# Optimization experiments

Measured on AMD Instinct MI355X. Metric: run time of the kernel, lower is better.

Reference implementation:

```python
import jax, jax.numpy as jnp
import numpy as np

NUM_HEADS = 16


def setup_inputs() -> dict:
    key = jax.random.key(0)
    ks = jax.random.split(key, 5)
    B, S, D = 2, 2048, 1024
    scale = 1.0 / np.sqrt(D)
    return {
        "hidden_states": jax.random.normal(ks[0], (B, S, D), dtype=jnp.float32),
        "Wq": jax.random.normal(ks[1], (D, D), dtype=jnp.float32) * scale,
        "bq": jnp.zeros((D,), jnp.float32),
        "Wk": jax.random.normal(ks[2], (D, D), dtype=jnp.float32) * scale,
        "bk": jnp.zeros((D,), jnp.float32),
        "Wv": jax.random.normal(ks[3], (D, D), dtype=jnp.float32) * scale,
        "bv": jnp.zeros((D,), jnp.float32),
        "Wo": jax.random.normal(ks[4], (D, D), dtype=jnp.float32) * scale,
        "bo": jnp.zeros((D,), jnp.float32),
    }


def reference(hidden_states, Wq, bq, Wk, bk, Wv, bv, Wo, bo):
    B, S, D = hidden_states.shape
    H = NUM_HEADS
    Dh = D // H

    def split_heads(x):  # [B,S,D] -> [B,H,S,Dh]
        return x.reshape(B, S, H, Dh).transpose(0, 2, 1, 3)

    q = split_heads(hidden_states @ Wq + bq)
    k = split_heads(hidden_states @ Wk + bk)
    v = split_heads(hidden_states @ Wv + bv)

    # causal additive mask: -inf strictly above the diagonal (triu, diagonal=1)
    i = jnp.arange(S)
    causal = jnp.where(i[None, :] > i[:, None], -jnp.inf, 0.0).astype(hidden_states.dtype)  # [S,S]

    scores = jnp.einsum("bhsd,bhtd->bhst", q, k) / jnp.sqrt(jnp.asarray(Dh, hidden_states.dtype))
    scores = scores + causal[None, None, :, :]
    weights = jax.nn.softmax(scores, axis=-1)  # [B,H,S,S]
    ctx = jnp.einsum("bhst,bhtd->bhsd", weights, v)
    ctx = ctx.transpose(0, 2, 1, 3).reshape(B, S, D)
    return ctx @ Wo + bo
```

## Files before the change

kernel.cpp:

```cpp
#include <hip/hip_runtime.h>
#include <math.h>

#define SEQ    2048
#define DMODEL 1024
#define NHEADS 16
#define DHEAD  64
#define NBATCH 2

typedef __attribute__((ext_vector_type(8)))  short bf16x8;
typedef __attribute__((ext_vector_type(4)))  float f32x4;
typedef __attribute__((ext_vector_type(16))) float f32x16;

__device__ __forceinline__ unsigned short f2bf(float f) {
    union { float f; unsigned u; } v; v.f = f;
    unsigned r = (v.u + 0x7FFF + ((v.u >> 16) & 1)) >> 16;
    return (unsigned short)r;
}

__device__ __forceinline__ unsigned cvt_pk_bf16(float lo, float hi) {
    unsigned r;
    asm("v_cvt_pk_bf16_f32 %0, %1, %2" : "=v"(r) : "v"(lo), "v"(hi));
    return r;
}

__device__ __forceinline__ void gload16(const void* g, void* l) {
    __builtin_amdgcn_global_load_lds(
        (const __attribute__((address_space(1))) unsigned*)g,
        (__attribute__((address_space(3))) unsigned*)l, 16, 0, 0);
}

__global__ __launch_bounds__(256)
void cast_bf16_kernel(const float* __restrict__ in, unsigned short* __restrict__ out) {
    const size_t g8 = ((size_t)blockIdx.x * 256 + threadIdx.x) * 8;
    float4 a = *reinterpret_cast<const float4*>(in + g8);
    float4 b = *reinterpret_cast<const float4*>(in + g8 + 4);
    bf16x8 o;
    o[0] = (short)f2bf(a.x); o[1] = (short)f2bf(a.y);
    o[2] = (short)f2bf(a.z); o[3] = (short)f2bf(a.w);
    o[4] = (short)f2bf(b.x); o[5] = (short)f2bf(b.y);
    o[6] = (short)f2bf(b.z); o[7] = (short)f2bf(b.w);
    *reinterpret_cast<bf16x8*>(out + g8) = o;
}

__global__ __launch_bounds__(256)
void wt_cast4_kernel(const float* __restrict__ W0, const float* __restrict__ W1,
                     const float* __restrict__ W2, const float* __restrict__ W3,
                     unsigned short* __restrict__ out) {
    __shared__ float tile[64][65];
    const int wsel = blockIdx.y;
    const float* W = (wsel == 0) ? W0 : (wsel == 1) ? W1 : (wsel == 2) ? W2 : W3;
    unsigned short* Wt = out + (size_t)wsel * 1024 * 1024;

    const int nt  = blockIdx.x & 15;
    const int kt  = blockIdx.x >> 4;
    const int tid = threadIdx.x;

#pragma unroll
    for (int r = 0; r < 4; ++r) {
        int kl = r * 16 + (tid >> 4);
        int nl = (tid & 15) * 4;
        float4 v = *reinterpret_cast<const float4*>(
            &W[(size_t)(kt * 64 + kl) * 1024 + nt * 64 + nl]);
        tile[kl][nl + 0] = v.x; tile[kl][nl + 1] = v.y;
        tile[kl][nl + 2] = v.z; tile[kl][nl + 3] = v.w;
    }
    __syncthreads();

    const int n  = tid >> 2;
    const int kc = (tid & 3) * 16;
    bf16x8 o0, o1;
#pragma unroll
    for (int i = 0; i < 8; ++i) o0[i] = (short)f2bf(tile[kc + i][n]);
#pragma unroll
    for (int i = 0; i < 8; ++i) o1[i] = (short)f2bf(tile[kc + 8 + i][n]);
    unsigned short* op = Wt + (size_t)(nt * 64 + n) * 1024 + kt * 64 + kc;
    *reinterpret_cast<bf16x8*>(op)     = o0;
    *reinterpret_cast<bf16x8*>(op + 8) = o1;
}

__global__ __launch_bounds__(256)
void vt_kernel(const unsigned short* __restrict__ Vh, unsigned short* __restrict__ Vt) {
    __shared__ unsigned short tile[64][72];
    const int bid = blockIdx.x;
    const int st  = bid & 31;
    const int bh  = bid >> 5;
    const int s0  = st * 64;
    const int tid = threadIdx.x;

    const int sl = tid >> 2;
    const int dc = (tid & 3) * 16;
    const unsigned short* src = Vh + ((size_t)bh * SEQ + s0 + sl) * 64 + dc;
    *reinterpret_cast<bf16x8*>(&tile[sl][dc])     = *reinterpret_cast<const bf16x8*>(src);
    *reinterpret_cast<bf16x8*>(&tile[sl][dc + 8]) = *reinterpret_cast<const bf16x8*>(src + 8);
    __syncthreads();

    const int dl = tid >> 2;
    const int sc = (tid & 3) * 16;
    unsigned short tmp[16];
#pragma unroll
    for (int k2 = 0; k2 < 16; ++k2) tmp[k2] = tile[sc + k2][dl];
    unsigned short* dst = Vt + ((size_t)bh * 64 + dl) * SEQ + s0 + sc;
    *reinterpret_cast<bf16x8*>(dst)     = *reinterpret_cast<bf16x8*>(&tmp[0]);
    *reinterpret_cast<bf16x8*>(dst + 8) = *reinterpret_cast<bf16x8*>(&tmp[8]);
}

template <int MODE>
__global__ __launch_bounds__(256)
void gemm_bf16(const unsigned short* __restrict__ A,
               const unsigned short* __restrict__ Bt,
               const float* __restrict__ bias0, const float* __restrict__ bias1,
               const float* __restrict__ bias2,
               float* __restrict__ Cf,
               unsigned short* __restrict__ Qo, unsigned short* __restrict__ Ko,
               unsigned short* __restrict__ Vo,
               int M, int N, int K) {
    __shared__ unsigned short As[2][128 * 32];
    __shared__ unsigned short Bs[2][128 * 32];

    int bx, by;
    {
        const int xcd = blockIdx.x & 7, i = blockIdx.x >> 3;
        if (MODE == 0) {
            bx = (xcd >> 2) * 12 + i % 12;
            by = (xcd & 3) * 8 + i / 12;
        } else {
            bx = (xcd & 1) * 4 + i % 4;
            by = (xcd >> 1) * 8 + i / 4;
        }
    }
    const int tid  = threadIdx.x;
    const int bm   = by * 128;
    const int bn   = bx * 128;
    const int w    = tid >> 6;
    const int lane = tid & 63;
    const int lrow = lane & 15;
    const int lk   = lane >> 4;
    const int wm0  = (w >> 1) * 64;
    const int wn0  = (w & 1) * 64;

    const int boff0 = tid * 16;
    const int boff1 = 4096 + tid * 16;
    const int row0  = tid >> 2;
    const int row1  = 64 + row0;
    const int c     = tid & 3;
    const int sw0   = (c ^ ((row0 >> 1) & 3)) * 8;
    const int sw1   = (c ^ ((row1 >> 1) & 3)) * 8;

    const unsigned short* Ag = A  + (size_t)bm * K;
    const unsigned short* Bg = Bt + (size_t)bn * K;

    f32x4 acc[4][4];
#pragma unroll
    for (int i = 0; i < 4; ++i)
#pragma unroll
        for (int j = 0; j < 4; ++j) acc[i][j] = (f32x4){0.f, 0.f, 0.f, 0.f};

    const int NT = K / 32;
    gload16(Ag + (size_t)row0 * K + sw0, (char*)&As[0][0] + boff0);
    gload16(Ag + (size_t)row1 * K + sw1, (char*)&As[0][0] + boff1);
    gload16(Bg + (size_t)row0 * K + sw0, (char*)&Bs[0][0] + boff0);
    gload16(Bg + (size_t)row1 * K + sw1, (char*)&Bs[0][0] + boff1);
    __syncthreads();

    int buf = 0;
    for (int kt = 0; kt < NT; ++kt) {
        if (kt + 1 < NT) {
            const int k0 = (kt + 1) * 32;
            gload16(Ag + (size_t)row0 * K + k0 + sw0, (char*)&As[buf ^ 1][0] + boff0);
            gload16(Ag + (size_t)row1 * K + k0 + sw1, (char*)&As[buf ^ 1][0] + boff1);
            gload16(Bg + (size_t)row0 * K + k0 + sw0, (char*)&Bs[buf ^ 1][0] + boff0);
            gload16(Bg + (size_t)row1 * K + k0 + sw1, (char*)&Bs[buf ^ 1][0] + boff1);
        }

        bf16x8 af[4], bf[4];
#pragma unroll
        for (int mg = 0; mg < 4; ++mg) {
            const int r = wm0 + mg * 16 + lrow;
            af[mg] = *reinterpret_cast<const bf16x8*>(
                (char*)&As[buf][0] + r * 64 + ((lk ^ ((r >> 1) & 3)) * 16));
        }
#pragma unroll
        for (int ng = 0; ng < 4; ++ng) {
            const int r = wn0 + ng * 16 + lrow;
            bf[ng] = *reinterpret_cast<const bf16x8*>(
                (char*)&Bs[buf][0] + r * 64 + ((lk ^ ((r >> 1) & 3)) * 16));
        }
#pragma unroll
        for (int mg = 0; mg < 4; ++mg)
#pragma unroll
            for (int ng = 0; ng < 4; ++ng)
                acc[mg][ng] = __builtin_amdgcn_mfma_f32_16x16x32_bf16(
                    af[mg], bf[ng], acc[mg][ng], 0, 0, 0);

        __syncthreads();
        buf ^= 1;
    }

    if (MODE == 0) {
        const int type = bn >> 10;
        const int nloc = bn & 1023;
        const float* bias = (type == 0) ? bias0 : (type == 1) ? bias1 : bias2;
        unsigned short* dst = (type == 0) ? Qo : (type == 1) ? Ko : Vo;
        const float scale = (type == 0) ? (0.125f * 1.44269504088896f) : 1.0f;
#pragma unroll
        for (int ng = 0; ng < 4; ++ng) {
            const int col = nloc + wn0 + ng * 16 + lrow;
            const float bv = bias[col];
            const int h = col >> 6, d = col & 63;
#pragma unroll
            for (int mg = 0; mg < 4; ++mg) {
#pragma unroll
                for (int j = 0; j < 4; ++j) {
                    const int row = bm + wm0 + mg * 16 + lk * 4 + j;
                    const int b = row >> 11, s = row & 2047;
                    const float val = (acc[mg][ng][j] + bv) * scale;
                    dst[((size_t)(b * 16 + h) * SEQ + s) * 64 + d] = f2bf(val);
                }
            }
        }
    } else {
#pragma unroll
        for (int ng = 0; ng < 4; ++ng) {
            const int col = bn + wn0 + ng * 16 + lrow;
            const float bv = bias0[col];
#pragma unroll
            for (int mg = 0; mg < 4; ++mg) {
#pragma unroll
                for (int j = 0; j < 4; ++j) {
                    const int row = bm + wm0 + mg * 16 + lk * 4 + j;
                    Cf[(size_t)row * N + col] = acc[mg][ng][j] + bv;
                }
            }
        }
    }
}

__global__ __launch_bounds__(256)
void attn_mfma_kernel(const unsigned short* __restrict__ Qg,
                      const unsigned short* __restrict__ Kg,
                      const unsigned short* __restrict__ Vtg,
                      unsigned short* __restrict__ CTX) {
    __shared__ __align__(16) unsigned short Ks[2][2][64 * 64];
    __shared__ __align__(16) unsigned short Vt[2][2][64 * 64];

    const int bid = blockIdx.x;
    const int xcd = bid & 7;
    const int s   = bid >> 3;
    const int bh  = xcd * 4 + (s & 3);
    const int k2  = s >> 2;
    const int rb  = (k2 < 8) ? k2 : (23 - k2);
    const int b  = bh >> 4;
    const int h  = bh & 15;
    const int r0 = rb * 128;
    const int tid  = threadIdx.x;
    const int w    = tid >> 6;
    const int lane = tid & 63;
    const int qcol = lane & 31;
    const int hlf  = lane >> 5;
    const int wr0  = r0 + w * 32;
    const int qrow = wr0 + qcol;

    const unsigned short* Kb = Kg + ((size_t)bh * SEQ) * DHEAD;
    const unsigned short* Vb = Vtg + ((size_t)bh * DHEAD) * SEQ;

    bf16x8 qf[4];
    {
        const unsigned short* qp = Qg + ((size_t)bh * SEQ + qrow) * DHEAD + hlf * 8;
#pragma unroll
        for (int ksub = 0; ksub < 4; ++ksub)
            qf[ksub] = *reinterpret_cast<const bf16x8*>(qp + ksub * 16);
    }

    f32x16 O0, O1;
#pragma unroll
    for (int r = 0; r < 16; ++r) { O0[r] = 0.f; O1[r] = 0.f; }
    float m = -1e30f, l = 0.f;

    const int srow = tid >> 2;
    const int c0   = (tid & 3) * 16;
    const int sb0  = srow * 128 + ((c0 * 2) ^ ((srow & 7) << 4));
    const int sb1  = srow * 128 + (((c0 + 8) * 2) ^ ((srow & 7) << 4));

    bf16x8 rk00, rk01, rk10, rk11, rv00, rv01, rv10, rv11;
    {
        const unsigned short* kp0 = Kb + (size_t)srow * DHEAD + c0;
        const unsigned short* kp1 = Kb + (size_t)(64 + srow) * DHEAD + c0;
        const unsigned short* vp  = Vb + (size_t)srow * SEQ + c0;
        rk00 = *reinterpret_cast<const bf16x8*>(kp0);
        rk01 = *reinterpret_cast<const bf16x8*>(kp0 + 8);
        rk10 = *reinterpret_cast<const bf16x8*>(kp1);
        rk11 = *reinterpret_cast<const bf16x8*>(kp1 + 8);
        rv00 = *reinterpret_cast<const bf16x8*>(vp);
        rv01 = *reinterpret_cast<const bf16x8*>(vp + 8);
        rv10 = *reinterpret_cast<const bf16x8*>(vp + 64);
        rv11 = *reinterpret_cast<const bf16x8*>(vp + 64 + 8);
    }

    const int nch = rb + 1;
    for (int ch = 0; ch < nch; ++ch) {
        const int jc  = ch * 128;
        const int buf = ch & 1;
        {
            char* k0 = (char*)&Ks[buf][0][0];
            char* k1 = (char*)&Ks[buf][1][0];
            char* v0 = (char*)&Vt[buf][0][0];
            char* v1 = (char*)&Vt[buf][1][0];
            *reinterpret_cast<bf16x8*>(k0 + sb0) = rk00;
            *reinterpret_cast<bf16x8*>(k0 + sb1) = rk01;
            *reinterpret_cast<bf16x8*>(k1 + sb0) = rk10;
            *reinterpret_cast<bf16x8*>(k1 + sb1) = rk11;
            *reinterpret_cast<bf16x8*>(v0 + sb0) = rv00;
            *reinterpret_cast<bf16x8*>(v0 + sb1) = rv01;
            *reinterpret_cast<bf16x8*>(v1 + sb0) = rv10;
            *reinterpret_cast<bf16x8*>(v1 + sb1) = rv11;
        }
        __syncthreads();
        if (ch + 1 < nch) {
            const int j1 = jc + 128;
            const unsigned short* kp0 = Kb + (size_t)(j1 + srow) * DHEAD + c0;
            const unsigned short* kp1 = Kb + (size_t)(j1 + 64 + srow) * DHEAD + c0;
            const unsigned short* vp  = Vb + (size_t)srow * SEQ + j1 + c0;
            rk00 = *reinterpret_cast<const bf16x8*>(kp0);
            rk01 = *reinterpret_cast<const bf16x8*>(kp0 + 8);
            rk10 = *reinterpret_cast<const bf16x8*>(kp1);
            rk11 = *reinterpret_cast<const bf16x8*>(kp1 + 8);
            rv00 = *reinterpret_cast<const bf16x8*>(vp);
            rv01 = *reinterpret_cast<const bf16x8*>(vp + 8);
            rv10 = *reinterpret_cast<const bf16x8*>(vp + 64);
            rv11 = *reinterpret_cast<const bf16x8*>(vp + 64 + 8);
        }

#pragma unroll
        for (int st = 0; st < 2; ++st) {
            const int j0 = jc + st * 64;
            if (j0 <= wr0 + 31) {
                const char* KB = (const char*)&Ks[buf][st][0];
                const char* VB = (const char*)&Vt[buf][st][0];
                f32x16 S[2];
#pragma unroll
                for (int r = 0; r < 16; ++r) { S[0][r] = 0.f; S[1][r] = 0.f; }
                __builtin_amdgcn_s_setprio(1);
#pragma unroll
                for (int kb = 0; kb < 2; ++kb) {
                    const int key = kb * 32 + qcol;
#pragma unroll
                    for (int ksub = 0; ksub < 4; ++ksub) {
                        int boff = key * 128 + ((ksub * 32 + hlf * 16) ^ ((key & 7) << 4));
                        bf16x8 kf = *reinterpret_cast<const bf16x8*>(KB + boff);
                        S[kb] = __builtin_amdgcn_mfma_f32_32x32x16_bf16(
                            kf, qf[ksub], S[kb], 0, 0, 0);
                    }
                }
                __builtin_amdgcn_s_setprio(0);

                if (j0 + 63 > wr0) {
#pragma unroll
                    for (int kb = 0; kb < 2; ++kb)
#pragma unroll
                        for (int r = 0; r < 16; ++r) {
                            int ka = j0 + kb * 32 + (r & 3) + 8 * (r >> 2) + 4 * hlf;
                            if (ka > qrow) S[kb][r] = -1e30f;
                        }
                }

                float mx[8];
#pragma unroll
                for (int r = 0; r < 8; ++r)
                    mx[r] = fmaxf(fmaxf(S[0][r], S[0][r + 8]),
                                  fmaxf(S[1][r], S[1][r + 8]));
                float m01 = fmaxf(mx[0], mx[1]), m23 = fmaxf(mx[2], mx[3]);
                float m45 = fmaxf(mx[4], mx[5]), m67 = fmaxf(mx[6], mx[7]);
                float pm = fmaxf(fmaxf(m01, m23), fmaxf(m45, m67));
                pm = fmaxf(pm, __shfl_xor(pm, 32));

                if (__any(pm > m)) {
                    float mnew = fmaxf(m, pm);
                    float cor  = __builtin_amdgcn_exp2f(m - mnew);
                    m = mnew;
                    l *= cor;
#pragma unroll
                    for (int r = 0; r < 16; ++r) { O0[r] *= cor; O1[r] *= cor; }
                }

                float l0 = 0.f, l1 = 0.f, l2 = 0.f, l3 = 0.f;
#pragma unroll
                for (int kb = 0; kb < 2; ++kb)
#pragma unroll
                    for (int r = 0; r < 16; r += 4) {
                        float p0 = __builtin_amdgcn_exp2f(S[kb][r + 0] - m);
                        float p1 = __builtin_amdgcn_exp2f(S[kb][r + 1] - m);
                        float p2 = __builtin_amdgcn_exp2f(S[kb][r + 2] - m);
                        float p3 = __builtin_amdgcn_exp2f(S[kb][r + 3] - m);
                        S[kb][r + 0] = p0; S[kb][r + 1] = p1;
                        S[kb][r + 2] = p2; S[kb][r + 3] = p3;
                        l0 += p0; l1 += p1; l2 += p2; l3 += p3;
                    }
                l += (l0 + l1) + (l2 + l3);

#pragma unroll
                for (int kc = 0; kc < 4; ++kc) {
                    const int kb = kc >> 1;
                    const int R0 = (kc & 1) * 8;
                    unsigned pa = cvt_pk_bf16(S[kb][R0 + 0], S[kb][R0 + 1]);
                    unsigned pc = cvt_pk_bf16(S[kb][R0 + 4], S[kb][R0 + 5]);
                    asm("v_permlane32_swap_b32 %0, %1" : "+v"(pa), "+v"(pc));
                    unsigned pb = cvt_pk_bf16(S[kb][R0 + 2], S[kb][R0 + 3]);
                    unsigned pd = cvt_pk_bf16(S[kb][R0 + 6], S[kb][R0 + 7]);
                    asm("v_permlane32_swap_b32 %0, %1" : "+v"(pb), "+v"(pd));
                    union { unsigned u[4]; bf16x8 v; } pf;
                    pf.u[0] = pa; pf.u[1] = pb; pf.u[2] = pc; pf.u[3] = pd;
                    __builtin_amdgcn_s_setprio(1);
#pragma unroll
                    for (int db = 0; db < 2; ++db) {
                        const int dim = db * 32 + qcol;
                        int boff = dim * 128 + ((kc * 32 + hlf * 16) ^ ((dim & 7) << 4));
                        bf16x8 vf = *reinterpret_cast<const bf16x8*>(VB + boff);
                        if (db == 0)
                            O0 = __builtin_amdgcn_mfma_f32_32x32x16_bf16(vf, pf.v, O0, 0, 0, 0);
                        else
                            O1 = __builtin_amdgcn_mfma_f32_32x32x16_bf16(vf, pf.v, O1, 0, 0, 0);
                    }
                    __builtin_amdgcn_s_setprio(0);
                }
            }
        }
    }

    l += __shfl_xor(l, 32);
    const float inv = 1.f / l;
    unsigned short* crow = CTX + ((size_t)(b * SEQ + qrow)) * DMODEL + h * DHEAD;
#pragma unroll
    for (int pq = 0; pq < 4; ++pq) {
        unsigned w0 = cvt_pk_bf16(O0[pq * 4 + 0] * inv, O0[pq * 4 + 1] * inv);
        unsigned w1 = cvt_pk_bf16(O0[pq * 4 + 2] * inv, O0[pq * 4 + 3] * inv);
        uint2 val; val.x = w0; val.y = w1;
        *reinterpret_cast<uint2*>(crow + 8 * pq + 4 * hlf) = val;
    }
#pragma unroll
    for (int pq = 0; pq < 4; ++pq) {
        unsigned w0 = cvt_pk_bf16(O1[pq * 4 + 0] * inv, O1[pq * 4 + 1] * inv);
        unsigned w1 = cvt_pk_bf16(O1[pq * 4 + 2] * inv, O1[pq * 4 + 3] * inv);
        uint2 val; val.x = w0; val.y = w1;
        *reinterpret_cast<uint2*>(crow + 32 + 8 * pq + 4 * hlf) = val;
    }
}

extern "C" void kernel_launch(void* const* d_in, const int* in_sizes, int n_in,
                              void* d_out, int out_size, void* d_ws, size_t ws_size,
                              hipStream_t stream) {
    const float* hs = (const float*)d_in[0];
    const float* Wq = (const float*)d_in[1];
    const float* bq = (const float*)d_in[2];
    const float* Wk = (const float*)d_in[3];
    const float* bk = (const float*)d_in[4];
    const float* Wv = (const float*)d_in[5];
    const float* bv = (const float*)d_in[6];
    const float* Wo = (const float*)d_in[7];
    const float* bo = (const float*)d_in[8];
    float* out = (float*)d_out;

    const size_t NTOK = (size_t)NBATCH * SEQ;
    unsigned short* hs_bf  = (unsigned short*)d_ws;
    unsigned short* Wqkv_t = hs_bf + NTOK * DMODEL;
    unsigned short* Wo_t   = Wqkv_t + 3072 * 1024;
    unsigned short* Qh     = Wo_t + 1024 * 1024;
    unsigned short* Kh     = Qh + NTOK * DMODEL;
    unsigned short* Vh     = Kh + NTOK * DMODEL;
    unsigned short* Vt     = Vh + NTOK * DMODEL;
    unsigned short* Cb     = Vt + NTOK * DMODEL;

    cast_bf16_kernel<<<(int)(NTOK * DMODEL / 8 / 256), 256, 0, stream>>>(hs, hs_bf);
    wt_cast4_kernel<<<dim3(256, 4), 256, 0, stream>>>(Wq, Wk, Wv, Wo, Wqkv_t);

    gemm_bf16<0><<<768, 256, 0, stream>>>(hs_bf, Wqkv_t, bq, bk, bv,
                                          nullptr, Qh, Kh, Vh,
                                          (int)NTOK, 3072, DMODEL);

    vt_kernel<<<1024, 256, 0, stream>>>(Vh, Vt);

    attn_mfma_kernel<<<NBATCH * NHEADS * (SEQ / 128), 256, 0, stream>>>(Qh, Kh, Vt, Cb);

    gemm_bf16<1><<<256, 256, 0, stream>>>(Cb, Wo_t, bo, nullptr, nullptr,
                                          out, nullptr, nullptr, nullptr,
                                          (int)NTOK, DMODEL, DMODEL);
}
```

Measured before the change: 121.9 us.

## Process both 64-key subtiles per softmax step and add lazy rescale threshold

Merges the two 64-key subtile iterations of the attention inner loop into one 128-key step: both QK^T MFMA blocks are issued before a single max/rescale/exp pass, then both PV blocks follow. This halves the number of cross-lane max reductions and rescale checks per chunk and gives the scheduler more independent MFMAs to overlap with softmax math. It also switches to a lazy rescale that only updates the running max when it grows by more than 8 (log2 units), skipping O/l rescaling in most steps at the cost of allowing exponent values up to 2^8. The wider step holds twice the score accumulators in registers, which raises VGPR pressure and may reduce occupancy or cause spills.

```diff
diff --git a/kernel.cpp b/kernel.cpp
--- a/kernel.cpp
+++ b/kernel.cpp
@@ -330,98 +330,169 @@
             rv11 = *reinterpret_cast<const bf16x8*>(vp + 64 + 8);
         }
 
-#pragma unroll
-        for (int st = 0; st < 2; ++st) {
-            const int j0 = jc + st * 64;
-            if (j0 <= wr0 + 31) {
-                const char* KB = (const char*)&Ks[buf][st][0];
-                const char* VB = (const char*)&Vt[buf][st][0];
-                f32x16 S[2];
-#pragma unroll
-                for (int r = 0; r < 16; ++r) { S[0][r] = 0.f; S[1][r] = 0.f; }
+        const bool v1ok = (jc + 64 <= wr0 + 31);
+        const char* KB0 = (const char*)&Ks[buf][0][0];
+        const char* KB1 = (const char*)&Ks[buf][1][0];
+        const char* VB0 = (const char*)&Vt[buf][0][0];
+        const char* VB1 = (const char*)&Vt[buf][1][0];
+
+        f32x16 S[4];
+#pragma unroll
+        for (int r = 0; r < 16; ++r) { S[0][r] = 0.f; S[1][r] = 0.f; }
+        __builtin_amdgcn_s_setprio(1);
+#pragma unroll
+        for (int kb = 0; kb < 2; ++kb) {
+            const int key = kb * 32 + qcol;
+#pragma unroll
+            for (int ksub = 0; ksub < 4; ++ksub) {
+                int boff = key * 128 + ((ksub * 32 + hlf * 16) ^ ((key & 7) << 4));
+                bf16x8 kf = *reinterpret_cast<const bf16x8*>(KB0 + boff);
+                S[kb] = __builtin_amdgcn_mfma_f32_32x32x16_bf16(
+                    kf, qf[ksub], S[kb], 0, 0, 0);
+            }
+        }
+        __builtin_amdgcn_s_setprio(0);
+        if (v1ok) {
+#pragma unroll
+            for (int r = 0; r < 16; ++r) { S[2][r] = 0.f; S[3][r] = 0.f; }
+            __builtin_amdgcn_s_setprio(1);
+#pragma unroll
+            for (int kb = 0; kb < 2; ++kb) {
+                const int key = kb * 32 + qcol;
+#pragma unroll
+                for (int ksub = 0; ksub < 4; ++ksub) {
+                    int boff = key * 128 + ((ksub * 32 + hlf * 16) ^ ((key & 7) << 4));
+                    bf16x8 kf = *reinterpret_cast<const bf16x8*>(KB1 + boff);
+                    S[2 + kb] = __builtin_amdgcn_mfma_f32_32x32x16_bf16(
+                        kf, qf[ksub], S[2 + kb], 0, 0, 0);
+                }
+            }
+            __builtin_amdgcn_s_setprio(0);
+        }
+
+        if (jc + 63 > wr0) {
+#pragma unroll
+            for (int kb = 0; kb < 2; ++kb)
+#pragma unroll
+                for (int r = 0; r < 16; ++r) {
+                    int ka = jc + kb * 32 + (r & 3) + 8 * (r >> 2) + 4 * hlf;
+                    if (ka > qrow) S[kb][r] = -1e30f;
+                }
+        }
+        if (v1ok && jc + 127 > wr0) {
+#pragma unroll
+            for (int kb = 0; kb < 2; ++kb)
+#pragma unroll
+                for (int r = 0; r < 16; ++r) {
+                    int ka = jc + 64 + kb * 32 + (r & 3) + 8 * (r >> 2) + 4 * hlf;
+                    if (ka > qrow) S[2 + kb][r] = -1e30f;
+                }
+        }
+
+        float mx[8];
+#pragma unroll
+        for (int r = 0; r < 8; ++r)
+            mx[r] = fmaxf(fmaxf(S[0][r], S[0][r + 8]),
+                          fmaxf(S[1][r], S[1][r + 8]));
+        if (v1ok) {
+#pragma unroll
+            for (int r = 0; r < 8; ++r)
+                mx[r] = fmaxf(mx[r], fmaxf(fmaxf(S[2][r], S[2][r + 8]),
+                                           fmaxf(S[3][r], S[3][r + 8])));
+        }
+        float m01 = fmaxf(mx[0], mx[1]), m23 = fmaxf(mx[2], mx[3]);
+        float m45 = fmaxf(mx[4], mx[5]), m67 = fmaxf(mx[6], mx[7]);
+        float pm = fmaxf(fmaxf(m01, m23), fmaxf(m45, m67));
+        pm = fmaxf(pm, __shfl_xor(pm, 32));
+
+        if (!__all(pm <= m + 8.f)) {
+            float mnew = fmaxf(m, pm);
+            float cor  = __builtin_amdgcn_exp2f(m - mnew);
+            m = mnew;
+            l *= cor;
+#pragma unroll
+            for (int r = 0; r < 16; ++r) { O0[r] *= cor; O1[r] *= cor; }
+        }
+
+        float l0 = 0.f, l1 = 0.f, l2 = 0.f, l3 = 0.f;
+#pragma unroll
+        for (int kb = 0; kb < 2; ++kb)
+#pragma unroll
+            for (int r = 0; r < 16; r += 4) {
+                float p0 = __builtin_amdgcn_exp2f(S[kb][r + 0] - m);
+                float p1 = __builtin_amdgcn_exp2f(S[kb][r + 1] - m);
+                float p2 = __builtin_amdgcn_exp2f(S[kb][r + 2] - m);
+                float p3 = __builtin_amdgcn_exp2f(S[kb][r + 3] - m);
+                S[kb][r + 0] = p0; S[kb][r + 1] = p1;
+                S[kb][r + 2] = p2; S[kb][r + 3] = p3;
+                l0 += p0; l1 += p1; l2 += p2; l3 += p3;
+            }
+        if (v1ok) {
+#pragma unroll
+            for (int kb = 2; kb < 4; ++kb)
+#pragma unroll
+                for (int r = 0; r < 16; r += 4) {
+                    float p0 = __builtin_amdgcn_exp2f(S[kb][r + 0] - m);
+                    float p1 = __builtin_amdgcn_exp2f(S[kb][r + 1] - m);
+                    float p2 = __builtin_amdgcn_exp2f(S[kb][r + 2] - m);
+                    float p3 = __builtin_amdgcn_exp2f(S[kb][r + 3] - m);
+                    S[kb][r + 0] = p0; S[kb][r + 1] = p1;
+                    S[kb][r + 2] = p2; S[kb][r + 3] = p3;
+                    l0 += p0; l1 += p1; l2 += p2; l3 += p3;
+                }
+        }
+        l += (l0 + l1) + (l2 + l3);
+
+#pragma unroll
+        for (int kc = 0; kc < 4; ++kc) {
+            const int kb = kc >> 1;
+            const int R0 = (kc & 1) * 8;
+            unsigned pa = cvt_pk_bf16(S[kb][R0 + 0], S[kb][R0 + 1]);
+            unsigned pc = cvt_pk_bf16(S[kb][R0 + 4], S[kb][R0 + 5]);
+            asm("v_permlane32_swap_b32 %0, %1" : "+v"(pa), "+v"(pc));
+            unsigned pb = cvt_pk_bf16(S[kb][R0 + 2], S[kb][R0 + 3]);
+            unsigned pd = cvt_pk_bf16(S[kb][R0 + 6], S[kb][R0 + 7]);
+            asm("v_permlane32_swap_b32 %0, %1" : "+v"(pb), "+v"(pd));
+            union { unsigned u[4]; bf16x8 v; } pf;
+            pf.u[0] = pa; pf.u[1] = pb; pf.u[2] = pc; pf.u[3] = pd;
+            __builtin_amdgcn_s_setprio(1);
+#pragma unroll
+            for (int db = 0; db < 2; ++db) {
+                const int dim = db * 32 + qcol;
+                int boff = dim * 128 + ((kc * 32 + hlf * 16) ^ ((dim & 7) << 4));
+                bf16x8 vf = *reinterpret_cast<const bf16x8*>(VB0 + boff);
+                if (db == 0)
+                    O0 = __builtin_amdgcn_mfma_f32_32x32x16_bf16(vf, pf.v, O0, 0, 0, 0);
+                else
+                    O1 = __builtin_amdgcn_mfma_f32_32x32x16_bf16(vf, pf.v, O1, 0, 0, 0);
+            }
+            __builtin_amdgcn_s_setprio(0);
+        }
+        if (v1ok) {
+#pragma unroll
+            for (int kc = 0; kc < 4; ++kc) {
+                const int kb = 2 + (kc >> 1);
+                const int R0 = (kc & 1) * 8;
+                unsigned pa = cvt_pk_bf16(S[kb][R0 + 0], S[kb][R0 + 1]);
+                unsigned pc = cvt_pk_bf16(S[kb][R0 + 4], S[kb][R0 + 5]);
+                asm("v_permlane32_swap_b32 %0, %1" : "+v"(pa), "+v"(pc));
+                unsigned pb = cvt_pk_bf16(S[kb][R0 + 2], S[kb][R0 + 3]);
+                unsigned pd = cvt_pk_bf16(S[kb][R0 + 6], S[kb][R0 + 7]);
+                asm("v_permlane32_swap_b32 %0, %1" : "+v"(pb), "+v"(pd));
+                union { unsigned u[4]; bf16x8 v; } pf;
+                pf.u[0] = pa; pf.u[1] = pb; pf.u[2] = pc; pf.u[3] = pd;
                 __builtin_amdgcn_s_setprio(1);
 #pragma unroll
-                for (int kb = 0; kb < 2; ++kb) {
-                    const int key = kb * 32 + qcol;
-#pragma unroll
-                    for (int ksub = 0; ksub < 4; ++ksub) {
-                        int boff = key * 128 + ((ksub * 32 + hlf * 16) ^ ((key & 7) << 4));
-                        bf16x8 kf = *reinterpret_cast<const bf16x8*>(KB + boff);
-                        S[kb] = __builtin_amdgcn_mfma_f32_32x32x16_bf16(
-                            kf, qf[ksub], S[kb], 0, 0, 0);
-                    }
+                for (int db = 0; db < 2; ++db) {
+                    const int dim = db * 32 + qcol;
+                    int boff = dim * 128 + ((kc * 32 + hlf * 16) ^ ((dim & 7) << 4));
+                    bf16x8 vf = *reinterpret_cast<const bf16x8*>(VB1 + boff);
+                    if (db == 0)
+                        O0 = __builtin_amdgcn_mfma_f32_32x32x16_bf16(vf, pf.v, O0, 0, 0, 0);
+                    else
+                        O1 = __builtin_amdgcn_mfma_f32_32x32x16_bf16(vf, pf.v, O1, 0, 0, 0);
                 }
                 __builtin_amdgcn_s_setprio(0);
-
-                if (j0 + 63 > wr0) {
-#pragma unroll
-                    for (int kb = 0; kb < 2; ++kb)
-#pragma unroll
-                        for (int r = 0; r < 16; ++r) {
-                            int ka = j0 + kb * 32 + (r & 3) + 8 * (r >> 2) + 4 * hlf;
-                            if (ka > qrow) S[kb][r] = -1e30f;
-                        }
-                }
-
-                float mx[8];
-#pragma unroll
-                for (int r = 0; r < 8; ++r)
-                    mx[r] = fmaxf(fmaxf(S[0][r], S[0][r + 8]),
-                                  fmaxf(S[1][r], S[1][r + 8]));
-                float m01 = fmaxf(mx[0], mx[1]), m23 = fmaxf(mx[2], mx[3]);
-                float m45 = fmaxf(mx[4], mx[5]), m67 = fmaxf(mx[6], mx[7]);
-                float pm = fmaxf(fmaxf(m01, m23), fmaxf(m45, m67));
-                pm = fmaxf(pm, __shfl_xor(pm, 32));
-
-                if (__any(pm > m)) {
-                    float mnew = fmaxf(m, pm);
-                    float cor  = __builtin_amdgcn_exp2f(m - mnew);
-                    m = mnew;
-                    l *= cor;
-#pragma unroll
-                    for (int r = 0; r < 16; ++r) { O0[r] *= cor; O1[r] *= cor; }
-                }
-
-                float l0 = 0.f, l1 = 0.f, l2 = 0.f, l3 = 0.f;
-#pragma unroll
-                for (int kb = 0; kb < 2; ++kb)
-#pragma unroll
-                    for (int r = 0; r < 16; r += 4) {
-                        float p0 = __builtin_amdgcn_exp2f(S[kb][r + 0] - m);
-                        float p1 = __builtin_amdgcn_exp2f(S[kb][r + 1] - m);
-                        float p2 = __builtin_amdgcn_exp2f(S[kb][r + 2] - m);
-                        float p3 = __builtin_amdgcn_exp2f(S[kb][r + 3] - m);
-                        S[kb][r + 0] = p0; S[kb][r + 1] = p1;
-                        S[kb][r + 2] = p2; S[kb][r + 3] = p3;
-                        l0 += p0; l1 += p1; l2 += p2; l3 += p3;
-                    }
-                l += (l0 + l1) + (l2 + l3);
-
-#pragma unroll
-                for (int kc = 0; kc < 4; ++kc) {
-                    const int kb = kc >> 1;
-                    const int R0 = (kc & 1) * 8;
-                    unsigned pa = cvt_pk_bf16(S[kb][R0 + 0], S[kb][R0 + 1]);
-                    unsigned pc = cvt_pk_bf16(S[kb][R0 + 4], S[kb][R0 + 5]);
-                    asm("v_permlane32_swap_b32 %0, %1" : "+v"(pa), "+v"(pc));
-                    unsigned pb = cvt_pk_bf16(S[kb][R0 + 2], S[kb][R0 + 3]);
-                    unsigned pd = cvt_pk_bf16(S[kb][R0 + 6], S[kb][R0 + 7]);
-                    asm("v_permlane32_swap_b32 %0, %1" : "+v"(pb), "+v"(pd));
-                    union { unsigned u[4]; bf16x8 v; } pf;
-                    pf.u[0] = pa; pf.u[1] = pb; pf.u[2] = pc; pf.u[3] = pd;
-                    __builtin_amdgcn_s_setprio(1);
-#pragma unroll
-                    for (int db = 0; db < 2; ++db) {
-                        const int dim = db * 32 + qcol;
-                        int boff = dim * 128 + ((kc * 32 + hlf * 16) ^ ((dim & 7) << 4));
-                        bf16x8 vf = *reinterpret_cast<const bf16x8*>(VB + boff);
-                        if (db == 0)
-                            O0 = __builtin_amdgcn_mfma_f32_32x32x16_bf16(vf, pf.v, O0, 0, 0, 0);
-                        else
-                            O1 = __builtin_amdgcn_mfma_f32_32x32x16_bf16(vf, pf.v, O1, 0, 0, 0);
-                    }
-                    __builtin_amdgcn_s_setprio(0);
-                }
             }
         }
     }
```

New measurement: 123.2 us. No clear change (+1.0%).

## Merge input and weight cast kernels; use lazy softmax rescale threshold

Applied to the files above, without the earlier changes.

Fuses the hidden-state bf16 cast and the four weight transpose-casts into one launch, selecting the work by block index, which saves one kernel launch and its tail. In attention, the running max is now updated only when a new max exceeds the old one by more than 8 in log2 units. This skips most rescaling of the O accumulators and l, at the cost of unnormalized exponentials up to 2^8, which fp32 handles safely.

```diff
diff --git a/kernel.cpp b/kernel.cpp
--- a/kernel.cpp
+++ b/kernel.cpp
@@ -30,30 +30,34 @@
 }
 
 __global__ __launch_bounds__(256)
-void cast_bf16_kernel(const float* __restrict__ in, unsigned short* __restrict__ out) {
-    const size_t g8 = ((size_t)blockIdx.x * 256 + threadIdx.x) * 8;
-    float4 a = *reinterpret_cast<const float4*>(in + g8);
-    float4 b = *reinterpret_cast<const float4*>(in + g8 + 4);
-    bf16x8 o;
-    o[0] = (short)f2bf(a.x); o[1] = (short)f2bf(a.y);
-    o[2] = (short)f2bf(a.z); o[3] = (short)f2bf(a.w);
-    o[4] = (short)f2bf(b.x); o[5] = (short)f2bf(b.y);
-    o[6] = (short)f2bf(b.z); o[7] = (short)f2bf(b.w);
-    *reinterpret_cast<bf16x8*>(out + g8) = o;
-}
-
-__global__ __launch_bounds__(256)
-void wt_cast4_kernel(const float* __restrict__ W0, const float* __restrict__ W1,
-                     const float* __restrict__ W2, const float* __restrict__ W3,
-                     unsigned short* __restrict__ out) {
+void prep_cast_kernel(const float* __restrict__ hs,
+                      const float* __restrict__ W0, const float* __restrict__ W1,
+                      const float* __restrict__ W2, const float* __restrict__ W3,
+                      unsigned short* __restrict__ hs_bf,
+                      unsigned short* __restrict__ Wt_out) {
     __shared__ float tile[64][65];
-    const int wsel = blockIdx.y;
+    const int bid = blockIdx.x;
+    const int tid = threadIdx.x;
+
+    if (bid < 2048) {
+        const size_t g8 = ((size_t)bid * 256 + tid) * 8;
+        float4 a = *reinterpret_cast<const float4*>(hs + g8);
+        float4 b = *reinterpret_cast<const float4*>(hs + g8 + 4);
+        bf16x8 o;
+        o[0] = (short)f2bf(a.x); o[1] = (short)f2bf(a.y);
+        o[2] = (short)f2bf(a.z); o[3] = (short)f2bf(a.w);
+        o[4] = (short)f2bf(b.x); o[5] = (short)f2bf(b.y);
+        o[6] = (short)f2bf(b.z); o[7] = (short)f2bf(b.w);
+        *reinterpret_cast<bf16x8*>(hs_bf + g8) = o;
+        return;
+    }
+
+    const int i    = bid - 2048;
+    const int wsel = i >> 8;
     const float* W = (wsel == 0) ? W0 : (wsel == 1) ? W1 : (wsel == 2) ? W2 : W3;
-    unsigned short* Wt = out + (size_t)wsel * 1024 * 1024;
-
-    const int nt  = blockIdx.x & 15;
-    const int kt  = blockIdx.x >> 4;
-    const int tid = threadIdx.x;
+    unsigned short* Wt = Wt_out + (size_t)wsel * 1024 * 1024;
+    const int nt = i & 15;
+    const int kt = (i >> 4) & 15;
 
 #pragma unroll
     for (int r = 0; r < 4; ++r) {
@@ -70,9 +74,9 @@
     const int kc = (tid & 3) * 16;
     bf16x8 o0, o1;
 #pragma unroll
-    for (int i = 0; i < 8; ++i) o0[i] = (short)f2bf(tile[kc + i][n]);
-#pragma unroll
-    for (int i = 0; i < 8; ++i) o1[i] = (short)f2bf(tile[kc + 8 + i][n]);
+    for (int i2 = 0; i2 < 8; ++i2) o0[i2] = (short)f2bf(tile[kc + i2][n]);
+#pragma unroll
+    for (int i2 = 0; i2 < 8; ++i2) o1[i2] = (short)f2bf(tile[kc + 8 + i2][n]);
     unsigned short* op = Wt + (size_t)(nt * 64 + n) * 1024 + kt * 64 + kc;
     *reinterpret_cast<bf16x8*>(op)     = o0;
     *reinterpret_cast<bf16x8*>(op + 8) = o1;
@@ -373,7 +377,7 @@
                 float pm = fmaxf(fmaxf(m01, m23), fmaxf(m45, m67));
                 pm = fmaxf(pm, __shfl_xor(pm, 32));
 
-                if (__any(pm > m)) {
+                if (!__all(pm <= m + 8.f)) {
                     float mnew = fmaxf(m, pm);
                     float cor  = __builtin_amdgcn_exp2f(m - mnew);
                     m = mnew;
@@ -469,8 +473,7 @@
     unsigned short* Vt     = Vh + NTOK * DMODEL;
     unsigned short* Cb     = Vt + NTOK * DMODEL;
 
-    cast_bf16_kernel<<<(int)(NTOK * DMODEL / 8 / 256), 256, 0, stream>>>(hs, hs_bf);
-    wt_cast4_kernel<<<dim3(256, 4), 256, 0, stream>>>(Wq, Wk, Wv, Wo, Wqkv_t);
+    prep_cast_kernel<<<3072, 256, 0, stream>>>(hs, Wq, Wk, Wv, Wo, hs_bf, Wqkv_t);
 
     gemm_bf16<0><<<768, 256, 0, stream>>>(hs_bf, Wqkv_t, bq, bk, bv,
                                           nullptr, Qh, Kh, Vh,
```

Measured after the change: 117.4 us. 3.7% less time.
